# Performance work log

Hardware: AMD Instinct MI355X
Metric: run time of the kernel (lower is better)

The kernel has to match this reference:

```python
import jax, jax.numpy as jnp
import numpy as np

N_WIRES = 10
DIM = 1 << N_WIRES          # 1024 amplitudes per token state
HIDDEN = 64                 # number of Pauli-Z-string measurements (= hidden_dim)
B, T = 8, 2048

# ops[k] = Z-string on qubits in bitmask (k+1): <psi|Z_mask|psi> = sum_i |psi_i|^2 * (-1)^popcount(i & mask)
_masks = np.arange(1, HIDDEN + 1, dtype=np.int64)
_ii = np.arange(DIM, dtype=np.int64)
_pc = (((_ii[None, :] & _masks[:, None])[..., None] >> np.arange(N_WIRES)) & 1).sum(-1)
SIGNS = jnp.asarray(1.0 - 2.0 * (_pc % 2), dtype=jnp.float32)   # (HIDDEN, DIM)

CNOT = jnp.array([[1, 0, 0, 0], [0, 1, 0, 0], [0, 0, 0, 1], [0, 0, 1, 0]], dtype=jnp.complex64)

def _rx(theta):
    c = jnp.cos(theta / 2).astype(jnp.complex64)
    s = jnp.sin(theta / 2).astype(jnp.complex64)
    return jnp.stack([jnp.stack([c, -1j * s]), jnp.stack([-1j * s, c])])

def _ry(theta):
    c = jnp.cos(theta / 2).astype(jnp.complex64)
    s = jnp.sin(theta / 2).astype(jnp.complex64)
    return jnp.stack([jnp.stack([c, -s]), jnp.stack([s, c])])

def _apply_1q(psi, g, j, n):
    # qubit 0 is the most-significant bit of the state index (matches expand_operator bit order)
    left, right = 1 << j, 1 << (n - 1 - j)
    p = psi.reshape(-1, left, 2, right)
    p = jnp.einsum('ab,mlbr->mlar', g, p)
    return p.reshape(-1, 1 << n)

def _apply_2q(psi, g, q0, q1, n):
    p = psi.reshape((-1,) + (2,) * n)
    p = jnp.moveaxis(p, (1 + q0, 1 + q1), (1, 2))
    p = jnp.einsum('abcd,mcd...->mab...', g.reshape(2, 2, 2, 2), p)
    p = jnp.moveaxis(p, (1, 2), (1 + q0, 1 + q1))
    return p.reshape(-1, 1 << n)

def _forward(x, rx0, ry0, ry1):
    n, dim = N_WIRES, DIM
    Bb, Tt, C = x.shape
    M = Bb * Tt
    # AmplitudeEncoder: zero-pad features to 2^n and L2-normalize
    psi = jnp.zeros((M, dim), jnp.complex64).at[:, :C].set(x.reshape(M, C).astype(jnp.complex64))
    nrm = jnp.sqrt(jnp.sum(psi.real**2 + psi.imag**2, axis=1, keepdims=True))
    psi = psi / nrm.astype(jnp.complex64)
    # U_total = (prod_j RY1_j) (prod_j CNOT_{j,(j+1)%n}) (prod_j RY0_j RX0_j), applied to psi.
    # Applying the gate sequence directly to the state == matmul with the expanded U_total.
    rx0_d = jax.lax.stop_gradient(rx0)  # original detaches RX params via .item()
    for j in range(n):
        psi = _apply_1q(psi, _rx(rx0_d[j]), j, n)
        psi = _apply_1q(psi, _ry(ry0[j]), j, n)
    for j in range(n):
        psi = _apply_2q(psi, CNOT, j, (j + 1) % n, n)
    for j in range(n):
        psi = _apply_1q(psi, _ry(ry1[j]), j, n)
    probs = psi.real**2 + psi.imag**2            # (M, DIM)
    out = probs @ SIGNS.T                        # (M, HIDDEN) Pauli-Z-string expectations
    return out.reshape(Bb, Tt, HIDDEN).astype(jnp.float32)

def setup_inputs():
    key = jax.random.key(0)
    k1, k2, k3, k4 = jax.random.split(key, 4)
    two_pi = 2.0 * float(np.pi)
    return {
        'x': jax.random.normal(k1, (B, T, HIDDEN), dtype=jnp.float32),
        'rx0': jax.random.uniform(k2, (N_WIRES,), dtype=jnp.float32, maxval=two_pi),
        'ry0': jax.random.uniform(k3, (N_WIRES,), dtype=jnp.float32, maxval=two_pi),
        'ry1': jax.random.uniform(k4, (N_WIRES,), dtype=jnp.float32, maxval=two_pi),
    }

def reference(x, rx0, ry0, ry1):
    return _forward(x, rx0, ry0, ry1)
```

## Files before the change

### kernel.cpp

```cpp
#include <hip/hip_runtime.h>

typedef __bf16 v8bf __attribute__((ext_vector_type(8)));
typedef float v4f __attribute__((ext_vector_type(4)));
typedef unsigned short u16x8 __attribute__((ext_vector_type(8)));

__device__ __forceinline__ unsigned short f2bf(float f) {
    unsigned int u = __float_as_uint(f);
    u += 0x7FFFu + ((u >> 16) & 1u);
    return (unsigned short)(u >> 16);
}

__device__ __forceinline__ v8bf ld_bf8(const unsigned short* p) {
    u16x8 r = *(const u16x8*)p;
    return __builtin_bit_cast(v8bf, r);
}

__device__ __forceinline__ float hw_cos(float h) {
    float r = h * 0.15915494309189535f, o;
    asm("v_cos_f32 %0, %1" : "=v"(o) : "v"(r));
    return o;
}
__device__ __forceinline__ float hw_sin(float h) {
    float r = h * 0.15915494309189535f, o;
    asm("v_sin_f32 %0, %1" : "=v"(o) : "v"(r));
    return o;
}

__global__ __launch_bounds__(64, 2) void build_V(
        const float* __restrict__ rx0, const float* __restrict__ ry0,
        const float* __restrict__ ry1,
        unsigned short* __restrict__ Vre, unsigned short* __restrict__ Vim)
{
    const int c = blockIdx.x;
    const int lane = threadIdx.x;

    float c1[10], s1[10];
    #pragma unroll
    for (int j = 0; j < 10; ++j) {
        float h = 0.5f * ry1[j];
        c1[j] = hw_cos(h); s1[j] = hw_sin(h);
    }

    int kk[16];
    #pragma unroll
    for (int q = 0; q < 16; ++q) {
        int k = lane + (q << 6);
        #pragma unroll
        for (int jj = 9; jj >= 0; --jj) {
            int cb = 9 - jj, tb = 9 - ((jj + 1) % 10);
            k ^= ((k >> cb) & 1) << tb;
        }
        kk[q] = k;
    }

    float ar[16], ai[16];
    #pragma unroll
    for (int q = 0; q < 16; ++q) { ar[q] = 1.f; ai[q] = 0.f; }

    #pragma unroll
    for (int j = 0; j < 10; ++j) {
        float hx = 0.5f * rx0[j], hy = 0.5f * ry0[j];
        float cx = hw_cos(hx), sx = hw_sin(hx), cy = hw_cos(hy), sy = hw_sin(hy);
        int cb = (c >> (9 - j)) & 1;
        float g0r = cb ? (-sy * cx) : (cy * cx);
        float g0i = cb ? (-cy * sx) : (sy * sx);
        float g1r = cb ? (cy * cx)  : (sy * cx);
        float g1i = cb ? (-sy * sx) : (-cy * sx);
        int p = 9 - j;
        #pragma unroll
        for (int q = 0; q < 16; ++q) {
            int kb = (kk[q] >> p) & 1;
            float fr = kb ? g1r : g0r;
            float fi = kb ? g1i : g0i;
            float nr = ar[q] * fr - ai[q] * fi;
            float ni = ar[q] * fi + ai[q] * fr;
            ar[q] = nr; ai[q] = ni;
        }
    }

    #pragma unroll
    for (int b = 0; b < 4; ++b) {
        float cy = c1[3 - b], sy = s1[3 - b];
        #pragma unroll
        for (int q = 0; q < 16; ++q) {
            if (q & (1 << b)) continue;
            int q2 = q | (1 << b);
            float A_r = ar[q], A_i = ai[q], B_r = ar[q2], B_i = ai[q2];
            ar[q]  = cy * A_r - sy * B_r;  ai[q]  = cy * A_i - sy * B_i;
            ar[q2] = sy * A_r + cy * B_r;  ai[q2] = sy * A_i + cy * B_i;
        }
    }
    #pragma unroll
    for (int p = 5; p >= 0; --p) {
        float cy = c1[9 - p], sy = s1[9 - p];
        int hi = (lane >> p) & 1;
        #pragma unroll
        for (int q = 0; q < 16; ++q) {
            float orr = __shfl_xor(ar[q], 1 << p);
            float oii = __shfl_xor(ai[q], 1 << p);
            ar[q] = hi ? (sy * orr + cy * ar[q]) : (cy * ar[q] - sy * orr);
            ai[q] = hi ? (sy * oii + cy * ai[q]) : (cy * ai[q] - sy * oii);
        }
    }

    #pragma unroll
    for (int q = 0; q < 16; ++q) {
        int i = lane + (q << 6);
        Vre[i * 64 + c] = f2bf(ar[q]);
        Vim[i * 64 + c] = f2bf(ai[q]);
    }
}

#define MFMA16(a, b, c) __builtin_amdgcn_mfma_f32_16x16x32_bf16(a, b, c, 0, 0, 0)

__global__ __launch_bounds__(256, 4) void qsa_fused(
        const float* __restrict__ x,
        const unsigned short* __restrict__ VS,
        float* __restrict__ out)
{
    __shared__ unsigned short vs[2][64][72];

    const int tid = threadIdx.x;
    const int w = tid >> 6, l = tid & 63;
    const int l15 = l & 15, lh = l >> 4;
    const int tb = blockIdx.x * 64 + w * 16;

    const int srow = tid >> 2;
    const int scol = (tid & 3) * 16;
    const unsigned short* sg = VS + srow * 64 + scol;

    const float* xrow = x + (size_t)(tb + l15) * 64;
    float4 v0 = *(const float4*)(xrow + lh * 8);
    float4 v1 = *(const float4*)(xrow + lh * 8 + 4);
    float4 v2 = *(const float4*)(xrow + 32 + lh * 8);
    float4 v3 = *(const float4*)(xrow + 32 + lh * 8 + 4);
    float ss = v0.x*v0.x + v0.y*v0.y + v0.z*v0.z + v0.w*v0.w
             + v1.x*v1.x + v1.y*v1.y + v1.z*v1.z + v1.w*v1.w
             + v2.x*v2.x + v2.y*v2.y + v2.z*v2.z + v2.w*v2.w
             + v3.x*v3.x + v3.y*v3.y + v3.z*v3.z + v3.w*v3.w;
    ss += __shfl_xor(ss, 16);
    ss += __shfl_xor(ss, 32);
    float rn = rsqrtf(ss);
    u16x8 ua0, ua1;
    ua0[0]=f2bf(v0.x*rn); ua0[1]=f2bf(v0.y*rn); ua0[2]=f2bf(v0.z*rn); ua0[3]=f2bf(v0.w*rn);
    ua0[4]=f2bf(v1.x*rn); ua0[5]=f2bf(v1.y*rn); ua0[6]=f2bf(v1.z*rn); ua0[7]=f2bf(v1.w*rn);
    ua1[0]=f2bf(v2.x*rn); ua1[1]=f2bf(v2.y*rn); ua1[2]=f2bf(v2.z*rn); ua1[3]=f2bf(v2.w*rn);
    ua1[4]=f2bf(v3.x*rn); ua1[5]=f2bf(v3.y*rn); ua1[6]=f2bf(v3.z*rn); ua1[7]=f2bf(v3.w*rn);
    const v8bf a0 = __builtin_bit_cast(v8bf, ua0);
    const v8bf a1 = __builtin_bit_cast(v8bf, ua1);

    float qE[4][4], qO[4][4];
    #pragma unroll
    for (int nb = 0; nb < 4; ++nb)
        #pragma unroll
        for (int rr = 0; rr < 4; ++rr) { qE[nb][rr] = 0.f; qO[nb][rr] = 0.f; }

    {
        u16x8 d0 = *(const u16x8*)(sg);
        u16x8 d1 = *(const u16x8*)(sg + 8);
        *(u16x8*)&vs[0][srow][scol] = d0;
        *(u16x8*)&vs[0][srow][scol + 8] = d1;
    }
    __syncthreads();

    #pragma unroll 2
    for (int p = 0; p < 32; ++p) {
        if (p + 1 < 32) {
            const unsigned short* gp = sg + (size_t)(p + 1) * 4096;
            u16x8 d0 = *(const u16x8*)(gp);
            u16x8 d1 = *(const u16x8*)(gp + 8);
            *(u16x8*)&vs[(p + 1) & 1][srow][scol] = d0;
            *(u16x8*)&vs[(p + 1) & 1][srow][scol + 8] = d1;
        }
        const unsigned short (*vb)[72] = vs[p & 1];
        #pragma unroll
        for (int nb = 0; nb < 4; ++nb) {
            v8bf b0 = ld_bf8(&vb[nb * 16 + l15][lh * 8]);
            v8bf b1 = ld_bf8(&vb[nb * 16 + l15][32 + lh * 8]);
            v4f z = (v4f){0.f, 0.f, 0.f, 0.f};
            v4f r = MFMA16(a0, b0, z);
            r     = MFMA16(a1, b1, r);
            if (p & 1) {
                #pragma unroll
                for (int rr = 0; rr < 4; ++rr) qO[nb][rr] += r[rr] * r[rr];
            } else {
                #pragma unroll
                for (int rr = 0; rr < 4; ++rr) qE[nb][rr] += r[rr] * r[rr];
            }
        }
        __syncthreads();
    }

    #pragma unroll
    for (int rr = 0; rr < 4; ++rr) {
        float w8[8];
        #pragma unroll
        for (int nb = 0; nb < 4; ++nb) { w8[nb] = qE[nb][rr]; w8[4 + nb] = qO[nb][rr]; }

        #pragma unroll
        for (int i = 0; i < 4; ++i) {
            float u = w8[i], v = w8[i + 4];
            w8[i] = u + v; w8[i + 4] = u - v;
        }
        #pragma unroll
        for (int g = 0; g < 8; g += 4)
            #pragma unroll
            for (int i = 0; i < 2; ++i) {
                float u = w8[g + i], v = w8[g + i + 2];
                w8[g + i] = u + v; w8[g + i + 2] = u - v;
            }
        #pragma unroll
        for (int g = 0; g < 8; g += 2) {
            float u = w8[g], v = w8[g + 1];
            w8[g] = u + v; w8[g + 1] = u - v;
        }
        #pragma unroll
        for (int st = 1; st <= 8; st <<= 1) {
            #pragma unroll
            for (int k = 0; k < 8; ++k) {
                float o = __shfl_xor(w8[k], st);
                w8[k] = (l15 & st) ? (o - w8[k]) : (w8[k] + o);
            }
        }
        float* orow = out + (size_t)(tb + lh * 4 + rr) * 64;
        #pragma unroll
        for (int nb = 0; nb < 4; ++nb)
            if (nb != 0 || l15 != 0) orow[nb * 16 + l15 - 1] = w8[nb];
        if (l15 == 0) orow[63] = w8[4];
    }
}

extern "C" void kernel_launch(void* const* d_in, const int* in_sizes, int n_in,
                              void* d_out, int out_size, void* d_ws, size_t ws_size,
                              hipStream_t stream) {
    const float* x   = (const float*)d_in[0];
    const float* rx0 = (const float*)d_in[1];
    const float* ry0 = (const float*)d_in[2];
    const float* ry1 = (const float*)d_in[3];
    float* out = (float*)d_out;

    unsigned short* Vre = (unsigned short*)d_ws;
    unsigned short* Vim = Vre + 1024 * 64;

    const int M = in_sizes[0] / 64;

    build_V<<<64, 64, 0, stream>>>(rx0, ry0, ry1, Vre, Vim);
    qsa_fused<<<M / 64, 256, 0, stream>>>(x, Vre, out);
}
```

Baseline: 88.60 us.

## Drop LDS staging; each wave loads V directly into registers with 4-deep prefetch

Replaces the 256-thread block that cooperatively staged V tiles through double-buffered shared memory with one-wave blocks. Each wave loads its MFMA B-operands straight from global memory (L2-resident) into four rotating register sets, issuing loads two chunks ahead of compute. This removes LDS writes/reads and per-chunk __syncthreads, at the cost of every wave re-reading the full V table from cache, quadrupling global/L2 traffic. It also raises register pressure and launches four times as many blocks.

Measured after the change: 106.9 us. 1.21x slower.

```diff
diff --git a/kernel.cpp b/kernel.cpp
--- a/kernel.cpp
+++ b/kernel.cpp
@@ -113,21 +113,41 @@
 
 #define MFMA16(a, b, c) __builtin_amdgcn_mfma_f32_16x16x32_bf16(a, b, c, 0, 0, 0)
 
-__global__ __launch_bounds__(256, 4) void qsa_fused(
+#define ISSUE(s, c) do {                                                     \
+    _Pragma("unroll")                                                        \
+    for (int _nb = 0; _nb < 4; ++_nb) {                                      \
+        s[_nb*2+0] = ld_bf8(vb + (size_t)(c) * 4096 + _nb * 1024);           \
+        s[_nb*2+1] = ld_bf8(vb + (size_t)(c) * 4096 + _nb * 1024 + 32);      \
+    }                                                                        \
+    __builtin_amdgcn_sched_barrier(0);                                       \
+    } while (0)
+
+#define COMP(s, q) do {                                                      \
+    _Pragma("unroll")                                                        \
+    for (int _nb = 0; _nb < 4; ++_nb) {                                      \
+        v4f _z = (v4f){0.f, 0.f, 0.f, 0.f};                                  \
+        v4f _r = MFMA16(a0, s[_nb*2+0], _z);                                 \
+        _r     = MFMA16(a1, s[_nb*2+1], _r);                                 \
+        _Pragma("unroll")                                                    \
+        for (int _rr = 0; _rr < 4; ++_rr)                                    \
+            q[_nb][_rr] += _r[_rr] * _r[_rr];                                \
+    } } while (0)
+
+#define GROUP(b) do {                                                        \
+    if ((b) + 2 < 32) ISSUE(sC, (b) + 2);  COMP(sA, qE);                     \
+    if ((b) + 3 < 32) ISSUE(sD, (b) + 3);  COMP(sB, qO);                     \
+    if ((b) + 4 < 32) ISSUE(sA, (b) + 4);  COMP(sC, qE);                     \
+    if ((b) + 5 < 32) ISSUE(sB, (b) + 5);  COMP(sD, qO);                     \
+    } while (0)
+
+__global__ __launch_bounds__(64) void qsa_fused(
         const float* __restrict__ x,
         const unsigned short* __restrict__ VS,
         float* __restrict__ out)
 {
-    __shared__ unsigned short vs[2][64][72];
-
-    const int tid = threadIdx.x;
-    const int w = tid >> 6, l = tid & 63;
+    const int l = threadIdx.x;
     const int l15 = l & 15, lh = l >> 4;
-    const int tb = blockIdx.x * 64 + w * 16;
-
-    const int srow = tid >> 2;
-    const int scol = (tid & 3) * 16;
-    const unsigned short* sg = VS + srow * 64 + scol;
+    const int tb = blockIdx.x * 16;
 
     const float* xrow = x + (size_t)(tb + l15) * 64;
     float4 v0 = *(const float4*)(xrow + lh * 8);
@@ -149,47 +169,20 @@
     const v8bf a0 = __builtin_bit_cast(v8bf, ua0);
     const v8bf a1 = __builtin_bit_cast(v8bf, ua1);
 
+    const unsigned short* vb = VS + (size_t)l15 * 64 + lh * 8;
+
     float qE[4][4], qO[4][4];
     #pragma unroll
     for (int nb = 0; nb < 4; ++nb)
         #pragma unroll
         for (int rr = 0; rr < 4; ++rr) { qE[nb][rr] = 0.f; qO[nb][rr] = 0.f; }
 
-    {
-        u16x8 d0 = *(const u16x8*)(sg);
-        u16x8 d1 = *(const u16x8*)(sg + 8);
-        *(u16x8*)&vs[0][srow][scol] = d0;
-        *(u16x8*)&vs[0][srow][scol + 8] = d1;
-    }
-    __syncthreads();
-
-    #pragma unroll 2
-    for (int p = 0; p < 32; ++p) {
-        if (p + 1 < 32) {
-            const unsigned short* gp = sg + (size_t)(p + 1) * 4096;
-            u16x8 d0 = *(const u16x8*)(gp);
-            u16x8 d1 = *(const u16x8*)(gp + 8);
-            *(u16x8*)&vs[(p + 1) & 1][srow][scol] = d0;
-            *(u16x8*)&vs[(p + 1) & 1][srow][scol + 8] = d1;
-        }
-        const unsigned short (*vb)[72] = vs[p & 1];
-        #pragma unroll
-        for (int nb = 0; nb < 4; ++nb) {
-            v8bf b0 = ld_bf8(&vb[nb * 16 + l15][lh * 8]);
-            v8bf b1 = ld_bf8(&vb[nb * 16 + l15][32 + lh * 8]);
-            v4f z = (v4f){0.f, 0.f, 0.f, 0.f};
-            v4f r = MFMA16(a0, b0, z);
-            r     = MFMA16(a1, b1, r);
-            if (p & 1) {
-                #pragma unroll
-                for (int rr = 0; rr < 4; ++rr) qO[nb][rr] += r[rr] * r[rr];
-            } else {
-                #pragma unroll
-                for (int rr = 0; rr < 4; ++rr) qE[nb][rr] += r[rr] * r[rr];
-            }
-        }
-        __syncthreads();
-    }
+    v8bf sA[8], sB[8], sC[8], sD[8];
+
+    ISSUE(sA, 0);
+    ISSUE(sB, 1);
+    GROUP(0);  GROUP(4);  GROUP(8);  GROUP(12);
+    GROUP(16); GROUP(20); GROUP(24); GROUP(28);
 
     #pragma unroll
     for (int rr = 0; rr < 4; ++rr) {
@@ -245,5 +238,5 @@
     const int M = in_sizes[0] / 64;
 
     build_V<<<64, 64, 0, stream>>>(rx0, ry0, ry1, Vre, Vim);
-    qsa_fused<<<M / 64, 256, 0, stream>>>(x, Vre, out);
-}
+    qsa_fused<<<M / 16, 64, 0, stream>>>(x, Vre, out);
+}
```
